# Kernel tuning notes

Hardware: AMD Instinct MI355X
Metric: run time of the kernel (lower is better)

Reference implementation:

```python
import jax, jax.numpy as jnp
import numpy as np

B, H, HKV, S, D = 2, 16, 4, 4096, 64
BN = 64            # block size (BLOCK_N)
G = 64             # num_global_tokens (== one block)
NB = S // BN       # total kv blocks
WINDOW = 3         # local window blocks per query block
NRAND = 3          # random blocks per query block
BPQ = WINDOW + NRAND
SCALE = 1.0 / float(np.sqrt(D))
NEG = -1e30


def setup_inputs() -> dict:
    key = jax.random.key(0)
    kq, kk, kv = jax.random.split(key, 3)
    q = jax.random.normal(kq, (B, H, S, D), jnp.float32)
    k = jax.random.normal(kk, (B, HKV, S, D), jnp.float32)
    v = jax.random.normal(kv, (B, HKV, S, D), jnp.float32)
    # 4 contiguous segments per batch row
    seg = jnp.arange(S, dtype=jnp.int32) // (S // 4)
    segment_ids = jnp.broadcast_to(seg, (B, S))
    alibi_slopes = jnp.asarray(2.0 ** (-8.0 * np.arange(1, H + 1) / H), jnp.float32)
    # block indices: per query block, window blocks + random blocks; -1 = skip
    rng = np.random.default_rng(0)
    bi = np.full((NB, BPQ), -1, np.int64)
    first = G // BN  # first sparse query block (global block handled separately)
    for i in range(first, NB):
        win = [b if first <= b < NB else -1 for b in (i - 1, i, i + 1)]
        rnd = rng.integers(first, NB, size=NRAND).tolist()
        bi[i] = win + rnd
    block_indices = jnp.asarray(bi)
    return {"q": q, "k": k, "v": v, "segment_ids": segment_ids,
            "block_indices": block_indices, "alibi_slopes": alibi_slopes}


def _softmax_attend(scores, values):
    m = jnp.max(scores, axis=-1, keepdims=True)
    p = jnp.exp(scores - m)
    l = jnp.sum(p, axis=-1, keepdims=True)
    l = jnp.where(l == 0.0, 1.0, l)
    return jnp.einsum('...qk,...kd->...qd', p / l, values)


def _forward(q, k, v, alibi_slopes, segment_ids, block_indices):
    hpg = H // HKV
    kf = jnp.repeat(k, hpg, axis=1)  # [B,H,S,D]
    vf = jnp.repeat(v, hpg, axis=1)
    pos = jnp.arange(S, dtype=jnp.float32)
    seg = segment_ids

    # ---- global queries: first G tokens attend to the full sequence ----
    qg = q[:, :, :G]
    sc_g = jnp.einsum('bhgd,bhsd->bhgs', qg, kf) * SCALE
    bias_g = -alibi_slopes[None, :, None, None] * jnp.abs(
        pos[:G][None, None, :, None] - pos[None, None, None, :])
    sc_g = sc_g + bias_g
    same_g = (seg[:, :G, None] == seg[:, None, :]) & (seg[:, :G, None] >= 0)
    sc_g = jnp.where(same_g[:, None], sc_g, NEG)
    out_g = _softmax_attend(sc_g, vf)  # [B,H,G,D]

    # ---- sparse query blocks: global KV + gathered window/random blocks ----
    first = G // BN
    nq = NB - first
    K = BPQ * BN
    qs = q[:, :, G:].reshape(B, H, nq, BN, D)
    bi = block_indices[first:]                      # [nq,BPQ]
    bi_safe = jnp.where(bi >= 0, bi, 0)
    kb = kf.reshape(B, H, NB, BN, D)[:, :, bi_safe].reshape(B, H, nq, K, D)
    vb = vf.reshape(B, H, NB, BN, D)[:, :, bi_safe].reshape(B, H, nq, K, D)
    kposi = (bi_safe * BN)[:, :, None] + jnp.arange(BN)      # [nq,BPQ,BN]
    valid = (jnp.broadcast_to((bi >= 0)[:, :, None], kposi.shape)
             & (kposi < S) & (kposi >= G)).reshape(nq, K)
    kposi = kposi.reshape(nq, K)
    kposf = kposi.astype(jnp.float32)
    qpos = jnp.arange(G, S, dtype=jnp.float32).reshape(nq, BN)
    qseg = seg[:, G:].reshape(B, nq, BN)
    kseg = seg[:, kposi]                            # [B,nq,K]

    sc_b = jnp.einsum('bhqmd,bhqnd->bhqmn', qs, kb) * SCALE
    sc_b = sc_b - alibi_slopes[None, :, None, None, None] * jnp.abs(
        qpos[:, :, None] - kposf[:, None, :])[None, None]
    same_b = (qseg[:, :, :, None] == kseg[:, :, None, :]) & (qseg[:, :, :, None] >= 0)
    sc_b = jnp.where((same_b & valid[None, :, None, :])[:, None], sc_b, NEG)

    gk, gv = kf[:, :, :G], vf[:, :, :G]
    sc_gk = jnp.einsum('bhqmd,bhgd->bhqmg', qs, gk) * SCALE
    sc_gk = sc_gk - alibi_slopes[None, :, None, None, None] * jnp.abs(
        qpos[:, :, None] - pos[:G][None, None, :])[None, None]
    gseg = seg[:, :G]
    same_gk = (qseg[:, :, :, None] == gseg[:, None, None, :]) & (qseg[:, :, :, None] >= 0)
    sc_gk = jnp.where(same_gk[:, None], sc_gk, NEG)

    scores = jnp.concatenate([sc_gk, sc_b], axis=-1)         # [B,H,nq,BN,G+K]
    vals = jnp.concatenate(
        [jnp.broadcast_to(gv[:, :, None], (B, H, nq, G, D)), vb], axis=-2)
    out_s = _softmax_attend(scores, vals).reshape(B, H, S - G, D)

    return jnp.concatenate([out_g, out_s], axis=2)           # [B,H,S,D]


def reference(q, k, v, segment_ids, block_indices, alibi_slopes):
    return _forward(q, k, v, alibi_slopes, segment_ids, block_indices)
```

## Files before the change

### kernel.cpp

```cpp
#include <hip/hip_runtime.h>
#include <hip/hip_bf16.h>

#define B_ 2
#define H_ 16
#define HKV_ 4
#define S_ 4096
#define D_ 64
#define BN_ 64
#define NB_ 64
#define BPQ_ 6
#define SCALE_ 0.125f
#define LDK 72
#define NSPLIT0 4
#define PART_ 4224

typedef short bf16x8 __attribute__((ext_vector_type(8)));
typedef short bf16x4v __attribute__((ext_vector_type(4)));
typedef float f32x4 __attribute__((ext_vector_type(4)));

static __device__ __forceinline__ short f2bf(float f) {
    unsigned u = __builtin_bit_cast(unsigned, f);
    unsigned r = u + 0x7FFFu + ((u >> 16) & 1u);
    return (short)(r >> 16);
}

__global__ __launch_bounds__(256) void sparse_attn_main(
    const float* __restrict__ q,
    const float* __restrict__ k,
    const float* __restrict__ v,
    const int* __restrict__ seg,
    const int* __restrict__ bidx,
    const float* __restrict__ slopes,
    float* __restrict__ out,
    float* __restrict__ ws)
{
    __shared__ short kc[BN_][LDK];
    __shared__ short vt[D_][LDK];
    __shared__ short pl[4][16][LDK];
    __shared__ int vlist[17];
    __shared__ int vcount;

    const int qbx  = blockIdx.x;
    int qb, split;
    if (qbx < NB_) { qb = qbx; split = 0; }
    else           { qb = 0;   split = qbx - (NB_ - 1); }
    const bool split_path = (qb == 0);

    const int bh   = blockIdx.y;
    const int b    = bh / H_;
    const int h    = bh % H_;
    const int hkv  = h / (H_ / HKV_);
    const int tid  = threadIdx.x;
    const int wave = tid >> 6;
    const int lane = tid & 63;
    const int l16  = lane & 15;
    const int lhi  = lane >> 4;

    const float slope = slopes[h];
    const int   qseg  = seg[b * S_ + qb * BN_];

    if (wave == 0) {
        const int n = split_path ? 16 : (1 + BPQ_);
        int cand = -1;
        if (lane < n) {
            if (split_path)       cand = split + 4 * lane;
            else if (lane == 0)   cand = 0;
            else                  cand = bidx[qb * BPQ_ + lane - 1];
        }
        bool ok = false;
        if (cand >= 0) {
            int ks_ = seg[b * S_ + cand * BN_];
            ok = (qseg >= 0) && (ks_ == qseg);
        }
        unsigned long long m = __ballot(ok);
        if (ok) {
            int rank = __popcll(m & ((1ull << lane) - 1ull));
            vlist[rank] = cand;
        }
        if (lane == 0) vcount = (int)__popcll(m);
    }

    const int qrow = qb * BN_ + wave * 16 + l16;
    const float* qp = q + (((size_t)(b * H_ + h)) * S_ + qrow) * D_;
    bf16x8 qf[2];
#pragma unroll
    for (int kk = 0; kk < 2; ++kk)
#pragma unroll
        for (int i = 0; i < 8; ++i)
            qf[kk][i] = f2bf(qp[kk * 32 + lhi * 8 + i]);

    f32x4 oacc[4] = {};
    float mrun[4], lrun[4];
#pragma unroll
    for (int r = 0; r < 4; ++r) { mrun[r] = -1e30f; lrun[r] = 0.f; }

    const float* kb_ptr = k + ((size_t)(b * HKV_ + hkv)) * S_ * D_;
    const float* vb_ptr = v + ((size_t)(b * HKV_ + hkv)) * S_ * D_;

    __syncthreads();
    const int nval = vcount;

    float4 kr0, kr1, kr2, kr3, vr0, vr1, vr2, vr3;
#define ISSUE_LOADS(CBLK) do { \
        const float4* ks_ = (const float4*)(kb_ptr + (size_t)(CBLK) * (BN_ * D_)); \
        const float4* vs_ = (const float4*)(vb_ptr + (size_t)(CBLK) * (BN_ * D_)); \
        kr0 = ks_[tid];       kr1 = ks_[tid + 256]; \
        kr2 = ks_[tid + 512]; kr3 = ks_[tid + 768]; \
        vr0 = vs_[tid];       vr1 = vs_[tid + 256]; \
        vr2 = vs_[tid + 512]; vr3 = vs_[tid + 768]; \
    } while (0)

#define WRITE_STAGE(IT, KR, VR) do { \
        int idx_ = tid + (IT) * 256; \
        int key_ = idx_ >> 4; \
        int d0_  = (idx_ & 15) * 4; \
        bf16x4v k4_ = { f2bf(KR.x), f2bf(KR.y), f2bf(KR.z), f2bf(KR.w) }; \
        *(bf16x4v*)&kc[key_][d0_] = k4_; \
        vt[d0_ + 0][key_] = f2bf(VR.x); \
        vt[d0_ + 1][key_] = f2bf(VR.y); \
        vt[d0_ + 2][key_] = f2bf(VR.z); \
        vt[d0_ + 3][key_] = f2bf(VR.w); \
    } while (0)

    if (nval > 0) ISSUE_LOADS(vlist[0]);

    for (int i = 0; i < nval; ++i) {
        const int kbase = vlist[i] * BN_;

        __syncthreads();
        WRITE_STAGE(0, kr0, vr0);
        WRITE_STAGE(1, kr1, vr1);
        WRITE_STAGE(2, kr2, vr2);
        WRITE_STAGE(3, kr3, vr3);
        if (i + 1 < nval) ISSUE_LOADS(vlist[i + 1]);
        __syncthreads();

        f32x4 sacc[4];
#pragma unroll
        for (int nt = 0; nt < 4; ++nt) {
            f32x4 s = {};
#pragma unroll
            for (int kk = 0; kk < 2; ++kk) {
                bf16x8 kf_ = *(const bf16x8*)&kc[nt * 16 + l16][kk * 32 + lhi * 8];
                s = __builtin_amdgcn_mfma_f32_16x16x32_bf16(qf[kk], kf_, s, 0, 0, 0);
            }
            sacc[nt] = s;
        }

        float pv_[4][4];
#pragma unroll
        for (int r = 0; r < 4; ++r) {
            const int m = lhi * 4 + r;
            const float qpos = (float)(qb * BN_ + wave * 16 + m);
            float mx = -1e30f;
#pragma unroll
            for (int nt = 0; nt < 4; ++nt) {
                float kpos = (float)(kbase + nt * 16 + l16);
                float sc = sacc[nt][r] * SCALE_ - slope * fabsf(qpos - kpos);
                pv_[nt][r] = sc;
                mx = fmaxf(mx, sc);
            }
            mx = fmaxf(mx, __shfl_xor(mx, 1));
            mx = fmaxf(mx, __shfl_xor(mx, 2));
            mx = fmaxf(mx, __shfl_xor(mx, 4));
            mx = fmaxf(mx, __shfl_xor(mx, 8));
            const float mn = fmaxf(mrun[r], mx);
            float sum = 0.f;
#pragma unroll
            for (int nt = 0; nt < 4; ++nt) {
                float p = __expf(pv_[nt][r] - mn);
                pv_[nt][r] = p;
                sum += p;
            }
            sum += __shfl_xor(sum, 1);
            sum += __shfl_xor(sum, 2);
            sum += __shfl_xor(sum, 4);
            sum += __shfl_xor(sum, 8);
            const float corr = __expf(mrun[r] - mn);
            mrun[r] = mn;
            lrun[r] = lrun[r] * corr + sum;
#pragma unroll
            for (int dt = 0; dt < 4; ++dt) oacc[dt][r] *= corr;
        }

#pragma unroll
        for (int r = 0; r < 4; ++r) {
            const int m = lhi * 4 + r;
#pragma unroll
            for (int nt = 0; nt < 4; ++nt)
                pl[wave][m][nt * 16 + l16] = f2bf(pv_[nt][r]);
        }

#pragma unroll
        for (int kk = 0; kk < 2; ++kk) {
            bf16x8 pf = *(const bf16x8*)&pl[wave][l16][kk * 32 + lhi * 8];
#pragma unroll
            for (int dt = 0; dt < 4; ++dt) {
                bf16x8 vf_ = *(const bf16x8*)&vt[dt * 16 + l16][kk * 32 + lhi * 8];
                oacc[dt] = __builtin_amdgcn_mfma_f32_16x16x32_bf16(pf, vf_, oacc[dt], 0, 0, 0);
            }
        }
    }

    if (split_path) {
        float* wsp = ws + (size_t)(bh * NSPLIT0 + split) * PART_;
#pragma unroll
        for (int r = 0; r < 4; ++r) {
            const int m = wave * 16 + lhi * 4 + r;
#pragma unroll
            for (int dt = 0; dt < 4; ++dt)
                wsp[m * D_ + dt * 16 + l16] = oacc[dt][r];
            if (l16 == 0) {
                wsp[4096 + m] = mrun[r];
                wsp[4160 + m] = lrun[r];
            }
        }
    } else {
        float* op = out + (((size_t)(b * H_ + h)) * S_ + qb * BN_ + wave * 16) * D_;
#pragma unroll
        for (int r = 0; r < 4; ++r) {
            const int m = lhi * 4 + r;
            const float inv = 1.0f / (lrun[r] == 0.f ? 1.f : lrun[r]);
#pragma unroll
            for (int dt = 0; dt < 4; ++dt)
                op[(size_t)m * D_ + dt * 16 + l16] = oacc[dt][r] * inv;
        }
    }
}

__global__ __launch_bounds__(256) void sparse_attn_combine(
    const float* __restrict__ ws,
    float* __restrict__ out)
{
    const int bh  = blockIdx.x;
    const int t   = threadIdx.x;
    const int row = t >> 2;
    const int d0  = (t & 3) * 16;

    const float* base = ws + (size_t)bh * NSPLIT0 * PART_;
    float ms[NSPLIT0], ls[NSPLIT0];
    float M = -1e30f;
#pragma unroll
    for (int s = 0; s < NSPLIT0; ++s) {
        ms[s] = base[s * PART_ + 4096 + row];
        ls[s] = base[s * PART_ + 4160 + row];
        M = fmaxf(M, ms[s]);
    }
    float w[NSPLIT0];
    float L = 0.f;
#pragma unroll
    for (int s = 0; s < NSPLIT0; ++s) {
        w[s] = __expf(ms[s] - M);
        L += w[s] * ls[s];
    }
    const float inv = 1.0f / (L == 0.f ? 1.f : L);

    float* op = out + ((size_t)bh * S_ + row) * D_ + d0;
#pragma unroll
    for (int j = 0; j < 16; ++j) {
        float acc = 0.f;
#pragma unroll
        for (int s = 0; s < NSPLIT0; ++s)
            acc += w[s] * base[s * PART_ + row * D_ + d0 + j];
        op[j] = acc * inv;
    }
}

extern "C" void kernel_launch(void* const* d_in, const int* in_sizes, int n_in,
                              void* d_out, int out_size, void* d_ws, size_t ws_size,
                              hipStream_t stream) {
    const float* q      = (const float*)d_in[0];
    const float* k      = (const float*)d_in[1];
    const float* v      = (const float*)d_in[2];
    const int*   seg    = (const int*)d_in[3];
    const int*   bidx   = (const int*)d_in[4];
    const float* slopes = (const float*)d_in[5];
    float*       out    = (float*)d_out;
    float*       ws     = (float*)d_ws;

    dim3 grid(NB_ + (NSPLIT0 - 1), B_ * H_);
    sparse_attn_main<<<grid, 256, 0, stream>>>(q, k, v, seg, bidx, slopes, out, ws);
    sparse_attn_combine<<<dim3(B_ * H_), 256, 0, stream>>>(ws, out);
}
```

Before: 152.6 us.

## Transpose score MFMA to keep P in registers and use exp2 softmax

Swaps the MFMA operand order so each lane holds one query row's scores. The row max and sum then need only two cross-lane shuffles, and P can be packed to bf16 in registers and fed straight into the PV MFMA, removing the per-wave LDS round trip for P. The softmax scale and log2e are folded into Q at load time so exp2f is used throughout, including in the combine kernel. It also XOR-swizzles the transposed V layout in LDS to cut bank conflicts and switches to float4 output stores. In exchange, the layout index arithmetic is more intricate and Q is rounded to bf16 after scaling.

```diff
diff --git a/kernel.cpp b/kernel.cpp
--- a/kernel.cpp
+++ b/kernel.cpp
@@ -9,7 +9,8 @@
 #define BN_ 64
 #define NB_ 64
 #define BPQ_ 6
-#define SCALE_ 0.125f
+#define QSCALE_LOG2 0.18033688f
+#define LOG2E 1.44269504f
 #define LDK 72
 #define NSPLIT0 4
 #define PART_ 4224
@@ -17,11 +18,18 @@
 typedef short bf16x8 __attribute__((ext_vector_type(8)));
 typedef short bf16x4v __attribute__((ext_vector_type(4)));
 typedef float f32x4 __attribute__((ext_vector_type(4)));
+typedef unsigned int u32x4 __attribute__((ext_vector_type(4)));
 
 static __device__ __forceinline__ short f2bf(float f) {
     unsigned u = __builtin_bit_cast(unsigned, f);
     unsigned r = u + 0x7FFFu + ((u >> 16) & 1u);
     return (short)(r >> 16);
+}
+
+static __device__ __forceinline__ unsigned cvt_pk_bf16(float lo, float hi) {
+    unsigned r;
+    asm("v_cvt_pk_bf16_f32 %0, %1, %2" : "=v"(r) : "v"(lo), "v"(hi));
+    return r;
 }
 
 __global__ __launch_bounds__(256) void sparse_attn_main(
@@ -36,7 +44,6 @@
 {
     __shared__ short kc[BN_][LDK];
     __shared__ short vt[D_][LDK];
-    __shared__ short pl[4][16][LDK];
     __shared__ int vlist[17];
     __shared__ int vcount;
 
@@ -56,8 +63,8 @@
     const int l16  = lane & 15;
     const int lhi  = lane >> 4;
 
-    const float slope = slopes[h];
-    const int   qseg  = seg[b * S_ + qb * BN_];
+    const float slope2 = slopes[h] * LOG2E;
+    const int   qseg   = seg[b * S_ + qb * BN_];
 
     if (wave == 0) {
         const int n = split_path ? 16 : (1 + BPQ_);
@@ -81,18 +88,17 @@
     }
 
     const int qrow = qb * BN_ + wave * 16 + l16;
+    const float qpos = (float)qrow;
     const float* qp = q + (((size_t)(b * H_ + h)) * S_ + qrow) * D_;
     bf16x8 qf[2];
 #pragma unroll
     for (int kk = 0; kk < 2; ++kk)
 #pragma unroll
         for (int i = 0; i < 8; ++i)
-            qf[kk][i] = f2bf(qp[kk * 32 + lhi * 8 + i]);
+            qf[kk][i] = f2bf(qp[kk * 32 + lhi * 8 + i] * QSCALE_LOG2);
 
     f32x4 oacc[4] = {};
-    float mrun[4], lrun[4];
-#pragma unroll
-    for (int r = 0; r < 4; ++r) { mrun[r] = -1e30f; lrun[r] = 0.f; }
+    float mrun = -1e30f, lrun = 0.f;
 
     const float* kb_ptr = k + ((size_t)(b * HKV_ + hkv)) * S_ * D_;
     const float* vb_ptr = v + ((size_t)(b * HKV_ + hkv)) * S_ * D_;
@@ -116,10 +122,11 @@
         int d0_  = (idx_ & 15) * 4; \
         bf16x4v k4_ = { f2bf(KR.x), f2bf(KR.y), f2bf(KR.z), f2bf(KR.w) }; \
         *(bf16x4v*)&kc[key_][d0_] = k4_; \
-        vt[d0_ + 0][key_] = f2bf(VR.x); \
-        vt[d0_ + 1][key_] = f2bf(VR.y); \
-        vt[d0_ + 2][key_] = f2bf(VR.z); \
-        vt[d0_ + 3][key_] = f2bf(VR.w); \
+        int sw_ = key_ ^ (((d0_ >> 2) & 7) << 3); \
+        vt[d0_ + 0][sw_] = f2bf(VR.x); \
+        vt[d0_ + 1][sw_] = f2bf(VR.y); \
+        vt[d0_ + 2][sw_] = f2bf(VR.z); \
+        vt[d0_ + 3][sw_] = f2bf(VR.w); \
     } while (0)
 
     if (nval > 0) ISSUE_LOADS(vlist[0]);
@@ -142,88 +149,86 @@
 #pragma unroll
             for (int kk = 0; kk < 2; ++kk) {
                 bf16x8 kf_ = *(const bf16x8*)&kc[nt * 16 + l16][kk * 32 + lhi * 8];
-                s = __builtin_amdgcn_mfma_f32_16x16x32_bf16(qf[kk], kf_, s, 0, 0, 0);
+                s = __builtin_amdgcn_mfma_f32_16x16x32_bf16(kf_, qf[kk], s, 0, 0, 0);
             }
             sacc[nt] = s;
         }
 
-        float pv_[4][4];
-#pragma unroll
-        for (int r = 0; r < 4; ++r) {
-            const int m = lhi * 4 + r;
-            const float qpos = (float)(qb * BN_ + wave * 16 + m);
-            float mx = -1e30f;
-#pragma unroll
-            for (int nt = 0; nt < 4; ++nt) {
-                float kpos = (float)(kbase + nt * 16 + l16);
-                float sc = sacc[nt][r] * SCALE_ - slope * fabsf(qpos - kpos);
-                pv_[nt][r] = sc;
+        float p_[4][4];
+        float mx = -1e30f;
+#pragma unroll
+        for (int nt = 0; nt < 4; ++nt)
+#pragma unroll
+            for (int r = 0; r < 4; ++r) {
+                float kpos = (float)(kbase + nt * 16 + lhi * 4 + r);
+                float sc = sacc[nt][r] - slope2 * fabsf(qpos - kpos);
+                p_[nt][r] = sc;
                 mx = fmaxf(mx, sc);
             }
-            mx = fmaxf(mx, __shfl_xor(mx, 1));
-            mx = fmaxf(mx, __shfl_xor(mx, 2));
-            mx = fmaxf(mx, __shfl_xor(mx, 4));
-            mx = fmaxf(mx, __shfl_xor(mx, 8));
-            const float mn = fmaxf(mrun[r], mx);
-            float sum = 0.f;
-#pragma unroll
-            for (int nt = 0; nt < 4; ++nt) {
-                float p = __expf(pv_[nt][r] - mn);
-                pv_[nt][r] = p;
+        mx = fmaxf(mx, __shfl_xor(mx, 16));
+        mx = fmaxf(mx, __shfl_xor(mx, 32));
+        const float mn = fmaxf(mrun, mx);
+        float sum = 0.f;
+#pragma unroll
+        for (int nt = 0; nt < 4; ++nt)
+#pragma unroll
+            for (int r = 0; r < 4; ++r) {
+                float p = exp2f(p_[nt][r] - mn);
+                p_[nt][r] = p;
                 sum += p;
             }
-            sum += __shfl_xor(sum, 1);
-            sum += __shfl_xor(sum, 2);
-            sum += __shfl_xor(sum, 4);
-            sum += __shfl_xor(sum, 8);
-            const float corr = __expf(mrun[r] - mn);
-            mrun[r] = mn;
-            lrun[r] = lrun[r] * corr + sum;
-#pragma unroll
-            for (int dt = 0; dt < 4; ++dt) oacc[dt][r] *= corr;
-        }
-
-#pragma unroll
-        for (int r = 0; r < 4; ++r) {
-            const int m = lhi * 4 + r;
-#pragma unroll
-            for (int nt = 0; nt < 4; ++nt)
-                pl[wave][m][nt * 16 + l16] = f2bf(pv_[nt][r]);
+        sum += __shfl_xor(sum, 16);
+        sum += __shfl_xor(sum, 32);
+        const float corr = exp2f(mrun - mn);
+        mrun = mn;
+        lrun = lrun * corr + sum;
+#pragma unroll
+        for (int dt = 0; dt < 4; ++dt) oacc[dt] *= corr;
+
+        unsigned pk_[4][2];
+#pragma unroll
+        for (int nt = 0; nt < 4; ++nt) {
+            pk_[nt][0] = cvt_pk_bf16(p_[nt][0], p_[nt][1]);
+            pk_[nt][1] = cvt_pk_bf16(p_[nt][2], p_[nt][3]);
         }
 
 #pragma unroll
         for (int kk = 0; kk < 2; ++kk) {
-            bf16x8 pf = *(const bf16x8*)&pl[wave][l16][kk * 32 + lhi * 8];
+            u32x4 pw = { pk_[2 * kk][0], pk_[2 * kk][1],
+                         pk_[2 * kk + 1][0], pk_[2 * kk + 1][1] };
+            bf16x8 pf = __builtin_bit_cast(bf16x8, pw);
 #pragma unroll
             for (int dt = 0; dt < 4; ++dt) {
-                bf16x8 vf_ = *(const bf16x8*)&vt[dt * 16 + l16][kk * 32 + lhi * 8];
-                oacc[dt] = __builtin_amdgcn_mfma_f32_16x16x32_bf16(pf, vf_, oacc[dt], 0, 0, 0);
+                const short* vrow = &vt[dt * 16 + l16][0];
+                const int sv8 = ((4 * dt + (l16 >> 2)) & 7) << 3;
+                bf16x4v lo = *(const bf16x4v*)&vrow[(kk * 32 + 4 * lhi) ^ sv8];
+                bf16x4v hi = *(const bf16x4v*)&vrow[(kk * 32 + 16 + 4 * lhi) ^ sv8];
+                bf16x8 vf = __builtin_shufflevector(lo, hi, 0, 1, 2, 3, 4, 5, 6, 7);
+                oacc[dt] = __builtin_amdgcn_mfma_f32_16x16x32_bf16(vf, pf, oacc[dt], 0, 0, 0);
             }
         }
     }
 
     if (split_path) {
         float* wsp = ws + (size_t)(bh * NSPLIT0 + split) * PART_;
-#pragma unroll
-        for (int r = 0; r < 4; ++r) {
-            const int m = wave * 16 + lhi * 4 + r;
-#pragma unroll
-            for (int dt = 0; dt < 4; ++dt)
-                wsp[m * D_ + dt * 16 + l16] = oacc[dt][r];
-            if (l16 == 0) {
-                wsp[4096 + m] = mrun[r];
-                wsp[4160 + m] = lrun[r];
-            }
+        const int m = wave * 16 + l16;
+#pragma unroll
+        for (int dt = 0; dt < 4; ++dt) {
+            float4 o4 = { oacc[dt][0], oacc[dt][1], oacc[dt][2], oacc[dt][3] };
+            *(float4*)&wsp[m * D_ + dt * 16 + 4 * lhi] = o4;
+        }
+        if (lhi == 0) {
+            wsp[4096 + m] = mrun;
+            wsp[4160 + m] = lrun;
         }
     } else {
-        float* op = out + (((size_t)(b * H_ + h)) * S_ + qb * BN_ + wave * 16) * D_;
-#pragma unroll
-        for (int r = 0; r < 4; ++r) {
-            const int m = lhi * 4 + r;
-            const float inv = 1.0f / (lrun[r] == 0.f ? 1.f : lrun[r]);
-#pragma unroll
-            for (int dt = 0; dt < 4; ++dt)
-                op[(size_t)m * D_ + dt * 16 + l16] = oacc[dt][r] * inv;
+        const float inv = 1.0f / (lrun == 0.f ? 1.f : lrun);
+        float* op = out + ((size_t)bh * S_ + qrow) * D_;
+#pragma unroll
+        for (int dt = 0; dt < 4; ++dt) {
+            float4 o4 = { oacc[dt][0] * inv, oacc[dt][1] * inv,
+                          oacc[dt][2] * inv, oacc[dt][3] * inv };
+            *(float4*)&op[dt * 16 + 4 * lhi] = o4;
         }
     }
 }
@@ -250,7 +255,7 @@
     float L = 0.f;
 #pragma unroll
     for (int s = 0; s < NSPLIT0; ++s) {
-        w[s] = __expf(ms[s] - M);
+        w[s] = exp2f(ms[s] - M);
         L += w[s] * ls[s];
     }
     const float inv = 1.0f / (L == 0.f ? 1.f : L);
```

New measurement: 139.5 us. -8.6%, faster.
